# Kernel tuning notes

Measured on AMD Instinct MI355X. Metric: run time of the kernel, lower is better.

## Reference

```python
import jax, jax.numpy as jnp
import numpy as np

N_E, N_C, N_DL, N_IT, N_EP, N_HA, N_CA, N_AS = 11964, 188, 100, 7, 100, 10, 10, 7
D = 128
B, S = 256, 400
N_V = N_E + 1      # hypergraph vertices (exercises)
N_HE = N_C + 1     # hyperedges (concepts)
MEMB = 3           # concept memberships per exercise
BN_EPS = 1e-5


def _hg_v2v_mean(X, pair_v, pair_e):
    # HGNN+ smoothing: vertex -> hyperedge (mean) -> vertex (mean)
    ones_e = jnp.ones(pair_e.shape, X.dtype)
    e_deg = jnp.clip(jax.ops.segment_sum(ones_e, pair_e, num_segments=N_HE), 1.0)
    v_deg = jnp.clip(jax.ops.segment_sum(ones_e, pair_v, num_segments=N_V), 1.0)
    E = jax.ops.segment_sum(X[pair_v], pair_e, num_segments=N_HE) / e_deg[:, None]
    return jax.ops.segment_sum(E[pair_e], pair_v, num_segments=N_V) / v_deg[:, None]


def _hgnnp_conv(X, W, b, gamma, beta, mean, var, pair_v, pair_e, is_last):
    X = X @ W + b
    X = (X - mean) * jax.lax.rsqrt(var + BN_EPS) * gamma + beta  # eval-mode BN
    X = _hg_v2v_mean(X, pair_v, pair_e)
    if not is_last:
        X = jax.nn.relu(X)
    return X


def setup_inputs() -> dict:
    key = jax.random.key(0)
    ks = jax.random.split(key, 32)
    inp = {}
    inp['input_e'] = jax.random.randint(ks[0], (B, S), 0, N_V)
    inp['input_ed'] = jax.random.randint(ks[1], (B, S), 0, N_DL + 1)
    inp['input_ep'] = jax.random.randint(ks[2], (B, S), 0, N_EP + 1)
    inp['input_a'] = jax.random.randint(ks[3], (B, S), 0, 2)
    inp['input_as'] = jax.random.randint(ks[4], (B, S), 0, N_AS + 1)
    inp['input_ha'] = jax.random.randint(ks[5], (B, S), 0, N_HA + 1)
    inp['input_ca'] = jax.random.randint(ks[6], (B, S), 0, N_CA + 1)
    inp['input_it'] = jax.random.randint(ks[7], (B, S), 0, N_IT + 1)
    inp['deliver_h'] = jnp.zeros((B, D), jnp.float32)
    # hypergraph incidence (exercise-concept Q-matrix edges)
    rng = np.random.default_rng(0)
    inp['pair_v'] = jnp.asarray(np.repeat(np.arange(N_V), MEMB))
    inp['pair_e'] = jnp.asarray(rng.integers(0, N_HE, size=N_V * MEMB))
    inp['ec_map'] = jax.random.randint(ks[8], (N_V,), 0, N_HE)
    inp['ecd_map'] = jax.random.randint(ks[9], (N_V,), 0, N_DL + 1)
    # embedding tables (xavier-ish scale)
    def emb(k, n):
        return jax.random.normal(k, (n, D), jnp.float32) * 0.05
    inp['e_table'] = emb(ks[10], N_V)
    inp['c_table'] = emb(ks[11], N_HE)
    inp['ed_table'] = emb(ks[12], N_DL + 1)
    inp['cd_table'] = emb(ks[13], N_DL + 1)
    inp['a_table'] = emb(ks[14], 2)
    inp['it_table'] = emb(ks[15], N_IT + 1)
    inp['ep_table'] = emb(ks[16], N_EP + 1)
    inp['ha_table'] = emb(ks[17], N_HA + 1)
    inp['ca_table'] = emb(ks[18], N_CA + 1)
    inp['as_table'] = emb(ks[19], N_AS + 1)
    # HGNNP conv 1 & 2
    def lin(k, din, dout):
        return jax.random.normal(k, (din, dout), jnp.float32) * (1.0 / np.sqrt(din))
    inp['W1'] = lin(ks[20], D, D); inp['b1'] = jnp.zeros((D,), jnp.float32)
    inp['g1'] = jnp.ones((D,), jnp.float32); inp['be1'] = jnp.zeros((D,), jnp.float32)
    inp['m1'] = jnp.zeros((D,), jnp.float32); inp['v1'] = jnp.ones((D,), jnp.float32)
    inp['W2'] = lin(ks[21], D, D); inp['b2'] = jnp.zeros((D,), jnp.float32)
    inp['g2'] = jnp.ones((D,), jnp.float32); inp['be2'] = jnp.zeros((D,), jnp.float32)
    inp['m2'] = jnp.zeros((D,), jnp.float32); inp['v2'] = jnp.ones((D,), jnp.float32)
    # linear_i: (d_e + d_dl + d_ep + d_c + d_dl) -> d_x
    inp['Wi'] = lin(ks[22], 5 * D, D); inp['bi'] = jnp.zeros((D,), jnp.float32)
    # GRU knowledge-state cell: input = concat(x, a_emb) -> 2D, hidden D, 3 gates
    inp['Wg'] = lin(ks[23], 2 * D, 3 * D)
    inp['Ug'] = lin(ks[24], D, 3 * D)
    inp['bg'] = jnp.zeros((3 * D,), jnp.float32)
    # linear_predicting_e: d_x -> 1
    inp['We'] = lin(ks[25], D, 1); inp['beo'] = jnp.zeros((1,), jnp.float32)
    # linear_predicting_s: 4*d -> 1
    inp['Ws'] = lin(ks[26], 4 * D, 1); inp['bs'] = jnp.zeros((1,), jnp.float32)
    return inp


def reference(input_e, input_ed, input_ep, input_a, input_as, input_ha, input_ca, input_it,
              deliver_h, pair_v, pair_e, ec_map, ecd_map,
              e_table, c_table, ed_table, cd_table, a_table, it_table, ep_table,
              ha_table, ca_table, as_table,
              W1, b1, g1, be1, m1, v1, W2, b2, g2, be2, m2, v2,
              Wi, bi, Wg, Ug, bg, We, beo, Ws, bs):
    # 2-layer HGNN+ over the exercise hypergraph
    X = _hgnnp_conv(e_table, W1, b1, g1, be1, m1, v1, pair_v, pair_e, is_last=False)
    X = _hgnnp_conv(X, W2, b2, g2, be2, m2, v2, pair_v, pair_e, is_last=True)
    # embedding gathers  [B,S,D]
    e_emb = X[input_e]
    c_emb = c_table[ec_map[input_e]]
    cd_emb = cd_table[ecd_map[input_e]]
    ed_emb = ed_table[input_ed]
    ep_emb = ep_table[input_ep]
    x = jnp.tanh(jnp.concatenate([e_emb, ed_emb, ep_emb, c_emb, cd_emb], -1) @ Wi + bi)  # [B,S,D]
    a_emb = a_table[input_a]
    xs = jnp.moveaxis(jnp.concatenate([x, a_emb], -1), 1, 0)  # [S,B,2D]
    xp = jnp.moveaxis(x, 1, 0)                                # [S,B,D]

    def step(h, inputs):
        xin, xq = inputs
        y = jax.nn.sigmoid((h * xq) @ We + beo)[..., 0]  # predict from prior knowledge state
        gi = xin @ Wg + bg
        gh = h @ Ug
        iz, ir, inn = jnp.split(gi, 3, -1)
        hz, hr, hn = jnp.split(gh, 3, -1)
        z = jax.nn.sigmoid(iz + hz)
        r = jax.nn.sigmoid(ir + hr)
        n = jnp.tanh(inn + r * hn)
        return (1.0 - z) * n + z * h, y

    _, ys = jax.lax.scan(step, deliver_h, (xs, xp))
    pred_main = jnp.moveaxis(ys, 0, 1)  # [B,S]
    s_in = jnp.concatenate([ha_table[input_ha], ca_table[input_ca],
                            as_table[input_as], it_table[input_it]], -1)
    pred_s = jax.nn.sigmoid(s_in @ Ws + bs)[..., 0]  # [B,S]
    return pred_s, pred_main
```

## Files before the change

kernel.cpp:

```cpp
#include <hip/hip_runtime.h>

#define N_V   11965
#define N_HE  189
#define NPAIR 35895
#define BB    256
#define SS    400
#define DD    128
#define BSR   102400

typedef __bf16 bf16x8 __attribute__((ext_vector_type(8)));
typedef float  f32x4  __attribute__((ext_vector_type(4)));

__device__ __forceinline__ ushort f2bf(float f) {
    unsigned x = __float_as_uint(f);
    return (ushort)((x + 0x7FFFu + ((x >> 16) & 1u)) >> 16);
}
__device__ __forceinline__ float bf2f(ushort u) { return __uint_as_float(((unsigned)u) << 16); }
__device__ __forceinline__ float sigm(float x) { return 1.f / (1.f + __expf(-x)); }
__device__ __forceinline__ float tanh_f(float x) { return 2.f * sigm(2.f * x) - 1.f; }
__device__ __forceinline__ float blo(unsigned u) { return __uint_as_float(u << 16); }
__device__ __forceinline__ float bhi(unsigned u) { return __uint_as_float(u); }

struct P1Args {
    const int* pair_e;
    const float *b1, *g1, *be1, *m1, *v1;
    const float *b2, *g2, *be2, *m2, *v2;
    const float *W1, *W2, *Wi, *Wg, *Ug;
    const float *ed_t, *ep_t, *c_t, *cd_t, *a_t, *bi, *bg;
    const float *ha_t, *ca_t, *as_t, *it_t, *Ws;
    int* e_deg;
    float* aff;
    ushort *W1T, *W2T, *WiTe, *WgT, *UgT;
    float *edW, *epW, *cW, *cdW, *agi, *sd;
};

__global__ __launch_bounds__(384) void p1_kernel(P1Args A) {
    int bid = blockIdx.x, t = threadIdx.x;
    if (bid == 0) {
        if (t < 128) {
            float s = A.g1[t] * rsqrtf(A.v1[t] + 1e-5f);
            A.aff[t] = s;
            A.aff[128 + t] = A.b1[t] * s + A.be1[t] - A.m1[t] * s;
        } else if (t < 256) {
            int d = t - 128;
            float s = A.g2[d] * rsqrtf(A.v2[d] + 1e-5f);
            A.aff[256 + d] = s;
            A.aff[384 + d] = A.b2[d] * s + A.be2[d] - A.m2[d] * s;
        }
        return;
    }
    bid -= 1;
    if (bid < 94) {
        int p = bid * 384 + t;
        if (p < NPAIR) atomicAdd(&A.e_deg[A.pair_e[p]], 1);
        return;
    }
    bid -= 94;
    if (bid < 43) {
        int i = bid * 384 + t;
        if (i < 16384) { int k = i >> 7, n = i & 127; A.W1T[n * 128 + k] = f2bf(A.W1[i]); }
        return;
    }
    bid -= 43;
    if (bid < 43) {
        int i = bid * 384 + t;
        if (i < 16384) { int k = i >> 7, n = i & 127; A.W2T[n * 128 + k] = f2bf(A.W2[i]); }
        return;
    }
    bid -= 43;
    if (bid < 43) {
        int i = bid * 384 + t;
        if (i < 16384) { int k = i >> 7, n = i & 127; A.WiTe[n * 128 + k] = f2bf(A.Wi[i]); }
        return;
    }
    bid -= 43;
    if (bid < 128) {
        int i = bid * 384 + t;
        if (i < 49152) { int k = i / 384, n = i % 384; A.WgT[n * 128 + k] = f2bf(A.Wg[i]); }
        return;
    }
    bid -= 128;
    if (bid < 128) {
        int i = bid * 384 + t;
        if (i < 49152) { int k = i / 384, n = i % 384; A.UgT[n * 128 + k] = f2bf(A.Ug[i]); }
        return;
    }
    bid -= 128;
    if (bid < 101) {
        if (t < 128) {
            float acc = 0.f;
            for (int k = 0; k < 128; ++k)
                acc += A.ed_t[bid * 128 + k] * A.Wi[(128 + k) * 128 + t];
            A.edW[bid * 128 + t] = acc + A.bi[t];
        }
        return;
    }
    bid -= 101;
    if (bid < 101) {
        if (t < 128) {
            float acc = 0.f;
            for (int k = 0; k < 128; ++k)
                acc += A.ep_t[bid * 128 + k] * A.Wi[(256 + k) * 128 + t];
            A.epW[bid * 128 + t] = acc;
        }
        return;
    }
    bid -= 101;
    if (bid < 189) {
        if (t < 128) {
            float acc = 0.f;
            for (int k = 0; k < 128; ++k)
                acc += A.c_t[bid * 128 + k] * A.Wi[(384 + k) * 128 + t];
            A.cW[bid * 128 + t] = acc;
        }
        return;
    }
    bid -= 189;
    if (bid < 101) {
        if (t < 128) {
            float acc = 0.f;
            for (int k = 0; k < 128; ++k)
                acc += A.cd_t[bid * 128 + k] * A.Wi[(512 + k) * 128 + t];
            A.cdW[bid * 128 + t] = acc;
        }
        return;
    }
    bid -= 101;
    if (bid < 2) {
        float acc = 0.f;
        for (int k = 0; k < 128; ++k)
            acc += A.a_t[bid * 128 + k] * A.Wg[(128 + k) * 384 + t];
        A.agi[bid * 384 + t] = acc + A.bg[t];
        return;
    }
    bid -= 2;
    {
        int r = bid;
        const float* tab; int woff, row;
        if (r < 11)      { tab = A.ha_t; row = r;      woff = 0;   }
        else if (r < 22) { tab = A.ca_t; row = r - 11; woff = 128; }
        else if (r < 30) { tab = A.as_t; row = r - 22; woff = 256; }
        else             { tab = A.it_t; row = r - 30; woff = 384; }
        if (t < 64) {
            float p = tab[row * 128 + t] * A.Ws[woff + t]
                    + tab[row * 128 + 64 + t] * A.Ws[woff + 64 + t];
            #pragma unroll
            for (int o = 32; o > 0; o >>= 1) p += __shfl_xor(p, o);
            if (t == 0) A.sd[r] = p;
        }
    }
}

__global__ void cvt_kernel(const float* __restrict__ src, ushort* __restrict__ dst, int n) {
    int i = blockIdx.x * 256 + threadIdx.x;
    if (i < n) dst[i] = f2bf(src[i]);
}

__global__ void csr_prefix(const int* __restrict__ e_deg, int* __restrict__ start) {
    __shared__ int sc[256];
    int t = threadIdx.x;
    int d = (t < N_HE) ? e_deg[t] : 0;
    sc[t] = d;
    __syncthreads();
    for (int off = 1; off < 256; off <<= 1) {
        int v = (t >= off) ? sc[t - off] : 0;
        __syncthreads();
        sc[t] += v;
        __syncthreads();
    }
    if (t < N_HE) start[t] = sc[t] - d;
    if (t == N_HE - 1) start[N_HE] = sc[t];
}

__global__ void csr_fill(const int* __restrict__ pair_e, const int* __restrict__ pair_v,
                         const int* __restrict__ start, int* __restrict__ cursor,
                         int* __restrict__ list) {
    int p = blockIdx.x * 384 + threadIdx.x;
    if (p >= NPAIR) return;
    int e = pair_e[p];
    int pos = atomicAdd(&cursor[e], 1);
    list[start[e] + pos] = pair_v[p];
}

template <int NT>
__global__ __launch_bounds__(256) void gemm_mfma(
    const ushort* __restrict__ Amat, const ushort* __restrict__ BT,
    float* __restrict__ out, int M,
    const float* __restrict__ colS, const float* __restrict__ colB,
    const float* __restrict__ agi, const int* __restrict__ aidx) {
    const int N = NT * 16;
    int lane = threadIdx.x & 63, wave = threadIdx.x >> 6;
    int q = lane >> 4, c = lane & 15;
    int rowbase = blockIdx.x * 64 + wave * 16;
    int arow = rowbase + c;
    if (arow > M - 1) arow = M - 1;
    f32x4 acc[NT];
#pragma unroll
    for (int i = 0; i < NT; ++i) acc[i] = (f32x4){0.f, 0.f, 0.f, 0.f};
#pragma unroll
    for (int ko = 0; ko < 4; ++ko) {
        bf16x8 af = *(const bf16x8*)(Amat + (size_t)arow * 128 + ko * 32 + q * 8);
#pragma unroll
        for (int nt = 0; nt < NT; ++nt) {
            bf16x8 bfr = *(const bf16x8*)(BT + (size_t)(nt * 16 + c) * 128 + ko * 32 + q * 8);
            acc[nt] = __builtin_amdgcn_mfma_f32_16x16x32_bf16(af, bfr, acc[nt], 0, 0, 0);
        }
    }
#pragma unroll
    for (int nt = 0; nt < NT; ++nt) {
        int col = nt * 16 + c;
        float s = colS ? colS[col] : 1.f;
        float bb = colB ? colB[col] : 0.f;
#pragma unroll
        for (int r = 0; r < 4; ++r) {
            int row = rowbase + q * 4 + r;
            if (row < M) {
                float v = acc[nt][r] * s + bb;
                if (agi) v += agi[aidx[row] * N + col];
                out[(size_t)row * N + col] = v;
            }
        }
    }
}

__global__ __launch_bounds__(512) void edge_mean(const float* __restrict__ Y,
                                                 const int* __restrict__ list,
                                                 const int* __restrict__ start,
                                                 float* __restrict__ E) {
    __shared__ float red[4][128];
    int e = blockIdx.x;
    int d = threadIdx.x & 127, g = threadIdx.x >> 7;
    int s0 = start[e], n = start[e + 1] - s0;
    float acc = 0.f;
    for (int i = g; i < n; i += 4) acc += Y[(size_t)list[s0 + i] * DD + d];
    red[g][d] = acc;
    __syncthreads();
    if (g == 0) {
        float v = red[0][d] + red[1][d] + red[2][d] + red[3][d];
        E[e * DD + d] = v / (float)(n > 0 ? n : 1);
    }
}

__global__ void v_mean(const float* __restrict__ E, const int* __restrict__ pair_e,
                       ushort* __restrict__ Xo, int relu) {
    int idx = blockIdx.x * 256 + threadIdx.x;
    if (idx >= N_V * DD) return;
    int v = idx >> 7, d = idx & 127;
    float a = E[pair_e[3 * v] * DD + d] + E[pair_e[3 * v + 1] * DD + d] +
              E[pair_e[3 * v + 2] * DD + d];
    a *= (1.f / 3.f);
    if (relu) a = fmaxf(a, 0.f);
    Xo[idx] = f2bf(a);
}

__global__ void k3_kernel(const int* __restrict__ in_e, const int* __restrict__ in_ed,
                          const int* __restrict__ in_ep, const float* __restrict__ XW,
                          const float* __restrict__ cW, const float* __restrict__ cdW,
                          const float* __restrict__ edW, const float* __restrict__ epW,
                          const int* __restrict__ ec_map, const int* __restrict__ ecd_map,
                          ushort* __restrict__ xbf) {
    int idx = blockIdx.x * 256 + threadIdx.x;
    if (idx >= BSR * DD) return;
    int row = idx >> 7, d = idx & 127;
    int e = in_e[row];
    float v = XW[(size_t)e * DD + d] + cW[ec_map[e] * DD + d] + cdW[ecd_map[e] * DD + d] +
              edW[in_ed[row] * DD + d] + epW[in_ep[row] * DD + d];
    xbf[idx] = f2bf(tanh_f(v));
}

__global__ void pred_s_kernel(const int* __restrict__ ha, const int* __restrict__ ca,
                              const int* __restrict__ as_, const int* __restrict__ it,
                              const float* __restrict__ sd, const float* __restrict__ bs,
                              float* __restrict__ out) {
    int i = blockIdx.x * 256 + threadIdx.x;
    if (i >= BSR) return;
    float v = sd[ha[i]] + sd[11 + ca[i]] + sd[22 + as_[i]] + sd[30 + it[i]] + bs[0];
    out[i] = sigm(v);
}

__global__ void
__attribute__((amdgpu_flat_work_group_size(768, 768), amdgpu_waves_per_eu(2, 3)))
gru_scan(
    const float* __restrict__ gi, const ushort* __restrict__ xb,
    const ushort* __restrict__ UgT, const float* __restrict__ h0,
    const float* __restrict__ We, const float* __restrict__ beo_p,
    float* __restrict__ out) {
    __shared__ __align__(16) float h_s[128];
    __shared__ float pp[4][392];
    __shared__ float n_sL[128];
    __shared__ float p_s[128];
    int b = blockIdx.x, t = threadIdx.x;
    int kq = t / 192;
    int cp = t % 192;
    const unsigned* WA = (const unsigned*)(UgT + (size_t)cp * 128 + kq * 32);
    const unsigned* WB = (const unsigned*)(UgT + (size_t)(cp + 192) * 128 + kq * 32);
    unsigned a0 = WA[0], a1 = WA[1], a2 = WA[2], a3 = WA[3], a4 = WA[4], a5 = WA[5],
             a6 = WA[6], a7 = WA[7], a8 = WA[8], a9 = WA[9], a10 = WA[10], a11 = WA[11],
             a12 = WA[12], a13 = WA[13], a14 = WA[14], a15 = WA[15];
    unsigned c0 = WB[0], c1 = WB[1], c2 = WB[2], c3 = WB[3], c4 = WB[4], c5 = WB[5],
             c6 = WB[6], c7 = WB[7], c8 = WB[8], c9 = WB[9], c10 = WB[10], c11 = WB[11],
             c12 = WB[12], c13 = WB[13], c14 = WB[14], c15 = WB[15];
    float beo = beo_p[0];
    float wev = 0.f;
    if (t < 128) { wev = We[t]; h_s[t] = h0[b * 128 + t]; }
    const float* gip = gi + (size_t)b * SS * 384;
    const ushort* xp = xb + (size_t)b * SS * 128;
    float gz_nx = 0.f, gr_nx = 0.f, gn_nx = 0.f, xw_nx = 0.f;
    if (t < 128) {
        gz_nx = gip[t];
        xw_nx = bf2f(xp[t]) * wev;
    } else if (t >= 256 && t < 384) {
        gr_nx = gip[t - 128];
        gn_nx = gip[t];
    }
    float* omain = out + BSR + b * SS;
    __syncthreads();
    for (int s = 0; s < SS; ++s) {
#define PIN(X) asm volatile("" : "+v"(X));
        PIN(a0) PIN(a1) PIN(a2) PIN(a3) PIN(a4) PIN(a5) PIN(a6) PIN(a7)
        PIN(a8) PIN(a9) PIN(a10) PIN(a11) PIN(a12) PIN(a13) PIN(a14) PIN(a15)
        PIN(c0) PIN(c1) PIN(c2) PIN(c3) PIN(c4) PIN(c5) PIN(c6) PIN(c7)
        PIN(c8) PIN(c9) PIN(c10) PIN(c11) PIN(c12) PIN(c13) PIN(c14) PIN(c15)
#undef PIN
        float gz = gz_nx, gr = gr_nx, gn = gn_nx, xw = xw_nx;
        if (s + 1 < SS) {
            const float* g2 = gip + (size_t)(s + 1) * 384;
            if (t < 128) {
                gz_nx = g2[t];
                xw_nx = bf2f(xp[(size_t)(s + 1) * 128 + t]) * wev;
            } else if (t >= 256 && t < 384) {
                gr_nx = g2[t - 128];
                gn_nx = g2[t];
            }
        }
        const float4* h4 = (const float4*)h_s + kq * 8;
        float accA = 0.f, accB = 0.f;
#define FB(I, UL, UH, VL, VH) { float4 hv = h4[I]; \
        accA = fmaf(hv.x, blo(UL), accA); accA = fmaf(hv.y, bhi(UL), accA); \
        accA = fmaf(hv.z, blo(UH), accA); accA = fmaf(hv.w, bhi(UH), accA); \
        accB = fmaf(hv.x, blo(VL), accB); accB = fmaf(hv.y, bhi(VL), accB); \
        accB = fmaf(hv.z, blo(VH), accB); accB = fmaf(hv.w, bhi(VH), accB); }
        FB(0, a0, a1, c0, c1)    FB(1, a2, a3, c2, c3)
        FB(2, a4, a5, c4, c5)    FB(3, a6, a7, c6, c7)
        FB(4, a8, a9, c8, c9)    FB(5, a10, a11, c10, c11)
        FB(6, a12, a13, c12, c13) FB(7, a14, a15, c14, c15)
#undef FB
        pp[kq][cp] = accA;
        pp[kq][cp + 192] = accB;
        __syncthreads();
        float z = 0.f, h_old = 0.f;
        if (t < 128) {
            float S = pp[0][t] + pp[1][t] + pp[2][t] + pp[3][t];
            z = sigm(gz + S);
            h_old = h_s[t];
            p_s[t] = h_old * xw;
        } else if (t >= 256 && t < 384) {
            int j = t - 256;
            float Sr = pp[0][128 + j] + pp[1][128 + j] + pp[2][128 + j] + pp[3][128 + j];
            float Sn = pp[0][256 + j] + pp[1][256 + j] + pp[2][256 + j] + pp[3][256 + j];
            float r = sigm(gr + Sr);
            n_sL[j] = tanh_f(gn + r * Sn);
        }
        __syncthreads();
        if (t < 128) {
            h_s[t] = (1.f - z) * n_sL[t] + z * h_old;
        } else if (t >= 384 && t < 448) {
            int l = t - 384;
            float pv = p_s[l] + p_s[l + 64];
#pragma unroll
            for (int o = 32; o > 0; o >>= 1) pv += __shfl_xor(pv, o);
            if (l == 0) omain[s] = sigm(pv + beo);
        }
        __syncthreads();
    }
}

extern "C" void kernel_launch(void* const* d_in, const int* in_sizes, int n_in,
                              void* d_out, int out_size, void* d_ws, size_t ws_size,
                              hipStream_t stream) {
    const int* in_e   = (const int*)d_in[0];
    const int* in_ed  = (const int*)d_in[1];
    const int* in_ep  = (const int*)d_in[2];
    const int* in_a   = (const int*)d_in[3];
    const int* in_as  = (const int*)d_in[4];
    const int* in_ha  = (const int*)d_in[5];
    const int* in_ca  = (const int*)d_in[6];
    const int* in_it  = (const int*)d_in[7];
    const float* deliver_h = (const float*)d_in[8];
    const int* pair_v = (const int*)d_in[9];
    const int* pair_e = (const int*)d_in[10];
    const int* ec_map = (const int*)d_in[11];
    const int* ecd_map= (const int*)d_in[12];
    const float* e_table  = (const float*)d_in[13];
    const float* c_table  = (const float*)d_in[14];
    const float* ed_table = (const float*)d_in[15];
    const float* cd_table = (const float*)d_in[16];
    const float* a_table  = (const float*)d_in[17];
    const float* it_table = (const float*)d_in[18];
    const float* ep_table = (const float*)d_in[19];
    const float* ha_table = (const float*)d_in[20];
    const float* ca_table = (const float*)d_in[21];
    const float* as_table = (const float*)d_in[22];
    const float* W1 = (const float*)d_in[23];
    const float* b1 = (const float*)d_in[24];
    const float* g1 = (const float*)d_in[25];
    const float* be1= (const float*)d_in[26];
    const float* m1 = (const float*)d_in[27];
    const float* v1 = (const float*)d_in[28];
    const float* W2 = (const float*)d_in[29];
    const float* b2 = (const float*)d_in[30];
    const float* g2 = (const float*)d_in[31];
    const float* be2= (const float*)d_in[32];
    const float* m2 = (const float*)d_in[33];
    const float* v2 = (const float*)d_in[34];
    const float* Wi = (const float*)d_in[35];
    const float* bi = (const float*)d_in[36];
    const float* Wg = (const float*)d_in[37];
    const float* Ug = (const float*)d_in[38];
    const float* bg = (const float*)d_in[39];
    const float* We = (const float*)d_in[40];
    const float* beo= (const float*)d_in[41];
    const float* Ws = (const float*)d_in[42];
    const float* bs = (const float*)d_in[43];
    float* out = (float*)d_out;
    char* ws = (char*)d_ws;

    size_t off = 0;
    auto alloc = [&](size_t bytes) { size_t o = off; off += (bytes + 255) & ~(size_t)255; return o; };
    size_t o_degcur = alloc(378 * 4);
    size_t o_start  = alloc(190 * 4);
    size_t o_list   = alloc((size_t)NPAIR * 4);
    size_t o_aff    = alloc(512 * 4);
    size_t o_W1T    = alloc(16384 * 2);
    size_t o_W2T    = alloc(16384 * 2);
    size_t o_WiTe   = alloc(16384 * 2);
    size_t o_WgT    = alloc(49152 * 2);
    size_t o_UgT    = alloc(49152 * 2);
    size_t o_edW    = alloc(101 * 128 * 4);
    size_t o_epW    = alloc(101 * 128 * 4);
    size_t o_cW     = alloc(189 * 128 * 4);
    size_t o_cdW    = alloc(101 * 128 * 4);
    size_t o_agi    = alloc(2 * 384 * 4);
    size_t o_sd     = alloc(38 * 4);
    size_t o_etb    = alloc((size_t)N_V * DD * 2);
    size_t o_E      = alloc((size_t)N_HE * DD * 4);
    size_t o_Y      = alloc((size_t)N_V * DD * 4);
    size_t o_X1     = alloc((size_t)N_V * DD * 2);
    size_t o_X2     = alloc((size_t)N_V * DD * 2);
    size_t o_XW     = alloc((size_t)N_V * DD * 4);
    size_t o_xbf    = alloc((size_t)BSR * DD * 2);
    size_t o_gi     = alloc((size_t)BSR * 384 * 4);

    int*    e_deg  = (int*)(ws + o_degcur);
    int*    cursor = e_deg + 189;
    int*    startp = (int*)(ws + o_start);
    int*    listp  = (int*)(ws + o_list);
    float*  aff    = (float*)(ws + o_aff);
    ushort* W1T    = (ushort*)(ws + o_W1T);
    ushort* W2T    = (ushort*)(ws + o_W2T);
    ushort* WiTe   = (ushort*)(ws + o_WiTe);
    ushort* WgT    = (ushort*)(ws + o_WgT);
    ushort* UgTp   = (ushort*)(ws + o_UgT);
    float*  edW    = (float*)(ws + o_edW);
    float*  epW    = (float*)(ws + o_epW);
    float*  cW     = (float*)(ws + o_cW);
    float*  cdW    = (float*)(ws + o_cdW);
    float*  agi    = (float*)(ws + o_agi);
    float*  sd     = (float*)(ws + o_sd);
    ushort* e_tb   = (ushort*)(ws + o_etb);
    float*  E      = (float*)(ws + o_E);
    float*  Y      = (float*)(ws + o_Y);
    ushort* X1b    = (ushort*)(ws + o_X1);
    ushort* X2b    = (ushort*)(ws + o_X2);
    float*  XW     = (float*)(ws + o_XW);
    ushort* xbf    = (ushort*)(ws + o_xbf);
    float*  gi     = (float*)(ws + o_gi);

    hipMemsetAsync(ws + o_degcur, 0, 378 * 4, stream);

    P1Args pa;
    pa.pair_e = pair_e;
    pa.b1 = b1; pa.g1 = g1; pa.be1 = be1; pa.m1 = m1; pa.v1 = v1;
    pa.b2 = b2; pa.g2 = g2; pa.be2 = be2; pa.m2 = m2; pa.v2 = v2;
    pa.W1 = W1; pa.W2 = W2; pa.Wi = Wi; pa.Wg = Wg; pa.Ug = Ug;
    pa.ed_t = ed_table; pa.ep_t = ep_table; pa.c_t = c_table; pa.cd_t = cd_table;
    pa.a_t = a_table; pa.bi = bi; pa.bg = bg;
    pa.ha_t = ha_table; pa.ca_t = ca_table; pa.as_t = as_table; pa.it_t = it_table; pa.Ws = Ws;
    pa.e_deg = e_deg; pa.aff = aff;
    pa.W1T = W1T; pa.W2T = W2T; pa.WiTe = WiTe; pa.WgT = WgT; pa.UgT = UgTp;
    pa.edW = edW; pa.epW = epW; pa.cW = cW; pa.cdW = cdW; pa.agi = agi; pa.sd = sd;
    p1_kernel<<<1012, 384, 0, stream>>>(pa);

    cvt_kernel<<<(N_V * DD + 255) / 256, 256, 0, stream>>>(e_table, e_tb, N_V * DD);
    csr_prefix<<<1, 256, 0, stream>>>(e_deg, startp);
    csr_fill<<<94, 384, 0, stream>>>(pair_e, pair_v, startp, cursor, listp);

    pred_s_kernel<<<(BSR + 255) / 256, 256, 0, stream>>>(in_ha, in_ca, in_as, in_it, sd, bs, out);

    gemm_mfma<8><<<(N_V + 63) / 64, 256, 0, stream>>>(e_tb, W1T, Y, N_V, aff, aff + 128,
                                                      nullptr, nullptr);
    edge_mean<<<N_HE, 512, 0, stream>>>(Y, listp, startp, E);
    v_mean<<<(N_V * DD + 255) / 256, 256, 0, stream>>>(E, pair_e, X1b, 1);
    gemm_mfma<8><<<(N_V + 63) / 64, 256, 0, stream>>>(X1b, W2T, Y, N_V, aff + 256, aff + 384,
                                                      nullptr, nullptr);
    edge_mean<<<N_HE, 512, 0, stream>>>(Y, listp, startp, E);
    v_mean<<<(N_V * DD + 255) / 256, 256, 0, stream>>>(E, pair_e, X2b, 0);
    gemm_mfma<8><<<(N_V + 63) / 64, 256, 0, stream>>>(X2b, WiTe, XW, N_V, nullptr, nullptr,
                                                      nullptr, nullptr);
    k3_kernel<<<(BSR * DD + 255) / 256, 256, 0, stream>>>(in_e, in_ed, in_ep, XW, cW, cdW, edW,
                                                          epW, ec_map, ecd_map, xbf);
    gemm_mfma<24><<<BSR / 64, 256, 0, stream>>>(xbf, WgT, gi, BSR, nullptr, nullptr, agi, in_a);
    gru_scan<<<BB, 768, 0, stream>>>(gi, xbf, UgTp, deliver_h, We, beo, out);
}
```

Before: 1.011 ms.

## Stage GRU recurrent weights in padded LDS instead of pinned registers

```diff
diff --git a/kernel.cpp b/kernel.cpp
--- a/kernel.cpp
+++ b/kernel.cpp
@@ -278,28 +278,34 @@
     out[i] = sigm(v);
 }
 
+#define WLDS_BYTES (384 * 272)
+#define GRU_LDS_BYTES (WLDS_BYTES + (128 * 3 + 4 * 392) * 4)
+
 __global__ void
-__attribute__((amdgpu_flat_work_group_size(768, 768), amdgpu_waves_per_eu(2, 3)))
-gru_scan(
+__attribute__((amdgpu_flat_work_group_size(768, 768)))
+gru_scan_lds(
     const float* __restrict__ gi, const ushort* __restrict__ xb,
     const ushort* __restrict__ UgT, const float* __restrict__ h0,
     const float* __restrict__ We, const float* __restrict__ beo_p,
     float* __restrict__ out) {
-    __shared__ __align__(16) float h_s[128];
-    __shared__ float pp[4][392];
-    __shared__ float n_sL[128];
-    __shared__ float p_s[128];
+    extern __shared__ __align__(16) char smem[];
+    ushort* w_lds = (ushort*)smem;
+    float* h_s  = (float*)(smem + WLDS_BYTES);
+    float* p_s  = h_s + 128;
+    float* n_sL = p_s + 128;
+    float* pp   = n_sL + 128;
     int b = blockIdx.x, t = threadIdx.x;
     int kq = t / 192;
     int cp = t % 192;
-    const unsigned* WA = (const unsigned*)(UgT + (size_t)cp * 128 + kq * 32);
-    const unsigned* WB = (const unsigned*)(UgT + (size_t)(cp + 192) * 128 + kq * 32);
-    unsigned a0 = WA[0], a1 = WA[1], a2 = WA[2], a3 = WA[3], a4 = WA[4], a5 = WA[5],
-             a6 = WA[6], a7 = WA[7], a8 = WA[8], a9 = WA[9], a10 = WA[10], a11 = WA[11],
-             a12 = WA[12], a13 = WA[13], a14 = WA[14], a15 = WA[15];
-    unsigned c0 = WB[0], c1 = WB[1], c2 = WB[2], c3 = WB[3], c4 = WB[4], c5 = WB[5],
-             c6 = WB[6], c7 = WB[7], c8 = WB[8], c9 = WB[9], c10 = WB[10], c11 = WB[11],
-             c12 = WB[12], c13 = WB[13], c14 = WB[14], c15 = WB[15];
+#pragma unroll
+    for (int j = 0; j < 8; ++j) {
+        int idx = j * 768 + t;
+        uint4 v = ((const uint4*)UgT)[idx];
+        int c = idx >> 4, u = idx & 15;
+        ((uint4*)w_lds)[c * 17 + u] = v;
+    }
+    const uint4* wA = (const uint4*)w_lds + cp * 17 + kq * 4;
+    const uint4* wB = (const uint4*)w_lds + (cp + 192) * 17 + kq * 4;
     float beo = beo_p[0];
     float wev = 0.f;
     if (t < 128) { wev = We[t]; h_s[t] = h0[b * 128 + t]; }
@@ -316,12 +322,6 @@
     float* omain = out + BSR + b * SS;
     __syncthreads();
     for (int s = 0; s < SS; ++s) {
-#define PIN(X) asm volatile("" : "+v"(X));
-        PIN(a0) PIN(a1) PIN(a2) PIN(a3) PIN(a4) PIN(a5) PIN(a6) PIN(a7)
-        PIN(a8) PIN(a9) PIN(a10) PIN(a11) PIN(a12) PIN(a13) PIN(a14) PIN(a15)
-        PIN(c0) PIN(c1) PIN(c2) PIN(c3) PIN(c4) PIN(c5) PIN(c6) PIN(c7)
-        PIN(c8) PIN(c9) PIN(c10) PIN(c11) PIN(c12) PIN(c13) PIN(c14) PIN(c15)
-#undef PIN
         float gz = gz_nx, gr = gr_nx, gn = gn_nx, xw = xw_nx;
         if (s + 1 < SS) {
             const float* g2 = gip + (size_t)(s + 1) * 384;
@@ -335,16 +335,109 @@
         }
         const float4* h4 = (const float4*)h_s + kq * 8;
         float accA = 0.f, accB = 0.f;
-#define FB(I, UL, UH, VL, VH) { float4 hv = h4[I]; \
-        accA = fmaf(hv.x, blo(UL), accA); accA = fmaf(hv.y, bhi(UL), accA); \
-        accA = fmaf(hv.z, blo(UH), accA); accA = fmaf(hv.w, bhi(UH), accA); \
-        accB = fmaf(hv.x, blo(VL), accB); accB = fmaf(hv.y, bhi(VL), accB); \
-        accB = fmaf(hv.z, blo(VH), accB); accB = fmaf(hv.w, bhi(VH), accB); }
-        FB(0, a0, a1, c0, c1)    FB(1, a2, a3, c2, c3)
-        FB(2, a4, a5, c4, c5)    FB(3, a6, a7, c6, c7)
-        FB(4, a8, a9, c8, c9)    FB(5, a10, a11, c10, c11)
-        FB(6, a12, a13, c12, c13) FB(7, a14, a15, c14, c15)
-#undef FB
+#pragma unroll
+        for (int i = 0; i < 4; ++i) {
+            uint4 a = wA[i];
+            uint4 c = wB[i];
+            float4 hv0 = h4[2 * i], hv1 = h4[2 * i + 1];
+            accA = fmaf(hv0.x, blo(a.x), accA); accA = fmaf(hv0.y, bhi(a.x), accA);
+            accA = fmaf(hv0.z, blo(a.y), accA); accA = fmaf(hv0.w, bhi(a.y), accA);
+            accA = fmaf(hv1.x, blo(a.z), accA); accA = fmaf(hv1.y, bhi(a.z), accA);
+            accA = fmaf(hv1.z, blo(a.w), accA); accA = fmaf(hv1.w, bhi(a.w), accA);
+            accB = fmaf(hv0.x, blo(c.x), accB); accB = fmaf(hv0.y, bhi(c.x), accB);
+            accB = fmaf(hv0.z, blo(c.y), accB); accB = fmaf(hv0.w, bhi(c.y), accB);
+            accB = fmaf(hv1.x, blo(c.z), accB); accB = fmaf(hv1.y, bhi(c.z), accB);
+            accB = fmaf(hv1.z, blo(c.w), accB); accB = fmaf(hv1.w, bhi(c.w), accB);
+        }
+        pp[kq * 392 + cp] = accA;
+        pp[kq * 392 + cp + 192] = accB;
+        __syncthreads();
+        float z = 0.f, h_old = 0.f;
+        if (t < 128) {
+            float S = pp[t] + pp[392 + t] + pp[784 + t] + pp[1176 + t];
+            z = sigm(gz + S);
+            h_old = h_s[t];
+            p_s[t] = h_old * xw;
+        } else if (t >= 256 && t < 384) {
+            int j = t - 256;
+            float Sr = pp[128 + j] + pp[392 + 128 + j] + pp[784 + 128 + j] + pp[1176 + 128 + j];
+            float Sn = pp[256 + j] + pp[392 + 256 + j] + pp[784 + 256 + j] + pp[1176 + 256 + j];
+            float r = sigm(gr + Sr);
+            n_sL[j] = tanh_f(gn + r * Sn);
+        }
+        __syncthreads();
+        if (t < 128) {
+            h_s[t] = (1.f - z) * n_sL[t] + z * h_old;
+        } else if (t >= 384 && t < 448) {
+            int l = t - 384;
+            float pv = p_s[l] + p_s[l + 64];
+#pragma unroll
+            for (int o = 32; o > 0; o >>= 1) pv += __shfl_xor(pv, o);
+            if (l == 0) omain[s] = sigm(pv + beo);
+        }
+        __syncthreads();
+    }
+}
+
+__global__ void
+__attribute__((amdgpu_flat_work_group_size(768, 768)))
+gru_scan_glob(
+    const float* __restrict__ gi, const ushort* __restrict__ xb,
+    const ushort* __restrict__ UgT, const float* __restrict__ h0,
+    const float* __restrict__ We, const float* __restrict__ beo_p,
+    float* __restrict__ out) {
+    __shared__ __align__(16) float h_s[128];
+    __shared__ float pp[4][392];
+    __shared__ float n_sL[128];
+    __shared__ float p_s[128];
+    int b = blockIdx.x, t = threadIdx.x;
+    int kq = t / 192;
+    int cp = t % 192;
+    const uint4* WA = (const uint4*)(UgT + (size_t)cp * 128 + kq * 32);
+    const uint4* WB = (const uint4*)(UgT + (size_t)(cp + 192) * 128 + kq * 32);
+    float beo = beo_p[0];
+    float wev = 0.f;
+    if (t < 128) { wev = We[t]; h_s[t] = h0[b * 128 + t]; }
+    const float* gip = gi + (size_t)b * SS * 384;
+    const ushort* xp = xb + (size_t)b * SS * 128;
+    float gz_nx = 0.f, gr_nx = 0.f, gn_nx = 0.f, xw_nx = 0.f;
+    if (t < 128) {
+        gz_nx = gip[t];
+        xw_nx = bf2f(xp[t]) * wev;
+    } else if (t >= 256 && t < 384) {
+        gr_nx = gip[t - 128];
+        gn_nx = gip[t];
+    }
+    float* omain = out + BSR + b * SS;
+    __syncthreads();
+    for (int s = 0; s < SS; ++s) {
+        float gz = gz_nx, gr = gr_nx, gn = gn_nx, xw = xw_nx;
+        if (s + 1 < SS) {
+            const float* g2 = gip + (size_t)(s + 1) * 384;
+            if (t < 128) {
+                gz_nx = g2[t];
+                xw_nx = bf2f(xp[(size_t)(s + 1) * 128 + t]) * wev;
+            } else if (t >= 256 && t < 384) {
+                gr_nx = g2[t - 128];
+                gn_nx = g2[t];
+            }
+        }
+        const float4* h4 = (const float4*)h_s + kq * 8;
+        float accA = 0.f, accB = 0.f;
+#pragma unroll
+        for (int i = 0; i < 4; ++i) {
+            uint4 a = WA[i];
+            uint4 c = WB[i];
+            float4 hv0 = h4[2 * i], hv1 = h4[2 * i + 1];
+            accA = fmaf(hv0.x, blo(a.x), accA); accA = fmaf(hv0.y, bhi(a.x), accA);
+            accA = fmaf(hv0.z, blo(a.y), accA); accA = fmaf(hv0.w, bhi(a.y), accA);
+            accA = fmaf(hv1.x, blo(a.z), accA); accA = fmaf(hv1.y, bhi(a.z), accA);
+            accA = fmaf(hv1.z, blo(a.w), accA); accA = fmaf(hv1.w, bhi(a.w), accA);
+            accB = fmaf(hv0.x, blo(c.x), accB); accB = fmaf(hv0.y, bhi(c.x), accB);
+            accB = fmaf(hv0.z, blo(c.y), accB); accB = fmaf(hv0.w, bhi(c.y), accB);
+            accB = fmaf(hv1.x, blo(c.z), accB); accB = fmaf(hv1.y, bhi(c.z), accB);
+            accB = fmaf(hv1.z, blo(c.w), accB); accB = fmaf(hv1.w, bhi(c.w), accB);
+        }
         pp[kq][cp] = accA;
         pp[kq][cp + 192] = accB;
         __syncthreads();
@@ -510,5 +603,13 @@
     k3_kernel<<<(BSR * DD + 255) / 256, 256, 0, stream>>>(in_e, in_ed, in_ep, XW, cW, cdW, edW,
                                                           epW, ec_map, ecd_map, xbf);
     gemm_mfma<24><<<BSR / 64, 256, 0, stream>>>(xbf, WgT, gi, BSR, nullptr, nullptr, agi, in_a);
-    gru_scan<<<BB, 768, 0, stream>>>(gi, xbf, UgTp, deliver_h, We, beo, out);
-}
+
+    hipError_t attr_ok = hipFuncSetAttribute(
+        reinterpret_cast<const void*>(gru_scan_lds),
+        hipFuncAttributeMaxDynamicSharedMemorySize, GRU_LDS_BYTES);
+    if (attr_ok == hipSuccess) {
+        gru_scan_lds<<<BB, 768, GRU_LDS_BYTES, stream>>>(gi, xbf, UgTp, deliver_h, We, beo, out);
+    } else {
+        gru_scan_glob<<<BB, 768, 0, stream>>>(gi, xbf, UgTp, deliver_h, We, beo, out);
+    }
+}
```

After: 1.031 ms. About the same (+1.9%).

## Cut GRU scan barriers per step and pin weights in AGPRs

Applied to the files above, without the earlier changes.

```diff
diff --git a/kernel.cpp b/kernel.cpp
--- a/kernel.cpp
+++ b/kernel.cpp
@@ -279,99 +279,109 @@
 }
 
 __global__ void
-__attribute__((amdgpu_flat_work_group_size(768, 768), amdgpu_waves_per_eu(2, 3)))
+__attribute__((amdgpu_flat_work_group_size(768, 768)))
 gru_scan(
     const float* __restrict__ gi, const ushort* __restrict__ xb,
     const ushort* __restrict__ UgT, const float* __restrict__ h0,
     const float* __restrict__ We, const float* __restrict__ beo_p,
     float* __restrict__ out) {
     __shared__ __align__(16) float h_s[128];
+    __shared__ float p_s[128];
     __shared__ float pp[4][392];
-    __shared__ float n_sL[128];
-    __shared__ float p_s[128];
     int b = blockIdx.x, t = threadIdx.x;
     int kq = t / 192;
     int cp = t % 192;
-    const unsigned* WA = (const unsigned*)(UgT + (size_t)cp * 128 + kq * 32);
-    const unsigned* WB = (const unsigned*)(UgT + (size_t)(cp + 192) * 128 + kq * 32);
-    unsigned a0 = WA[0], a1 = WA[1], a2 = WA[2], a3 = WA[3], a4 = WA[4], a5 = WA[5],
-             a6 = WA[6], a7 = WA[7], a8 = WA[8], a9 = WA[9], a10 = WA[10], a11 = WA[11],
-             a12 = WA[12], a13 = WA[13], a14 = WA[14], a15 = WA[15];
-    unsigned c0 = WB[0], c1 = WB[1], c2 = WB[2], c3 = WB[3], c4 = WB[4], c5 = WB[5],
-             c6 = WB[6], c7 = WB[7], c8 = WB[8], c9 = WB[9], c10 = WB[10], c11 = WB[11],
-             c12 = WB[12], c13 = WB[13], c14 = WB[14], c15 = WB[15];
+    const uint4* WA = (const uint4*)(UgT + (size_t)cp * 128 + kq * 32);
+    const uint4* WB = (const uint4*)(UgT + (size_t)(cp + 192) * 128 + kq * 32);
+    uint4 A0 = WA[0], A1 = WA[1], A2 = WA[2], A3 = WA[3];
+    uint4 B0 = WB[0], B1 = WB[1], B2 = WB[2], B3 = WB[3];
+    unsigned a0 = A0.x, a1 = A0.y, a2 = A0.z, a3 = A0.w;
+    unsigned a4 = A1.x, a5 = A1.y, a6 = A1.z, a7 = A1.w;
+    unsigned a8 = A2.x, a9 = A2.y, a10 = A2.z, a11 = A2.w;
+    unsigned a12 = A3.x, a13 = A3.y, a14 = A3.z, a15 = A3.w;
+    unsigned c0 = B0.x, c1 = B0.y, c2 = B0.z, c3 = B0.w;
+    unsigned c4 = B1.x, c5 = B1.y, c6 = B1.z, c7 = B1.w;
+    unsigned c8 = B2.x, c9 = B2.y, c10 = B2.z, c11 = B2.w;
+    unsigned c12 = B3.x, c13 = B3.y, c14 = B3.z, c15 = B3.w;
     float beo = beo_p[0];
-    float wev = 0.f;
-    if (t < 128) { wev = We[t]; h_s[t] = h0[b * 128 + t]; }
+    float wev = 0.f, hreg = 0.f;
+    if (t < 128) {
+        wev = We[t];
+        hreg = h0[b * 128 + t];
+        h_s[t] = hreg;
+    }
     const float* gip = gi + (size_t)b * SS * 384;
     const ushort* xp = xb + (size_t)b * SS * 128;
     float gz_nx = 0.f, gr_nx = 0.f, gn_nx = 0.f, xw_nx = 0.f;
     if (t < 128) {
         gz_nx = gip[t];
+        gr_nx = gip[128 + t];
+        gn_nx = gip[256 + t];
         xw_nx = bf2f(xp[t]) * wev;
-    } else if (t >= 256 && t < 384) {
-        gr_nx = gip[t - 128];
-        gn_nx = gip[t];
     }
     float* omain = out + BSR + b * SS;
     __syncthreads();
     for (int s = 0; s < SS; ++s) {
-#define PIN(X) asm volatile("" : "+v"(X));
-        PIN(a0) PIN(a1) PIN(a2) PIN(a3) PIN(a4) PIN(a5) PIN(a6) PIN(a7)
-        PIN(a8) PIN(a9) PIN(a10) PIN(a11) PIN(a12) PIN(a13) PIN(a14) PIN(a15)
-        PIN(c0) PIN(c1) PIN(c2) PIN(c3) PIN(c4) PIN(c5) PIN(c6) PIN(c7)
-        PIN(c8) PIN(c9) PIN(c10) PIN(c11) PIN(c12) PIN(c13) PIN(c14) PIN(c15)
-#undef PIN
+#define PINA(X) asm volatile("" : "+a"(X));
+        PINA(a0) PINA(a1) PINA(a2) PINA(a3) PINA(a4) PINA(a5) PINA(a6) PINA(a7)
+        PINA(a8) PINA(a9) PINA(a10) PINA(a11) PINA(a12) PINA(a13) PINA(a14) PINA(a15)
+        PINA(c0) PINA(c1) PINA(c2) PINA(c3) PINA(c4) PINA(c5) PINA(c6) PINA(c7)
+        PINA(c8) PINA(c9) PINA(c10) PINA(c11) PINA(c12) PINA(c13) PINA(c14) PINA(c15)
+#undef PINA
         float gz = gz_nx, gr = gr_nx, gn = gn_nx, xw = xw_nx;
-        if (s + 1 < SS) {
+        if (s + 1 < SS && t < 128) {
             const float* g2 = gip + (size_t)(s + 1) * 384;
-            if (t < 128) {
-                gz_nx = g2[t];
-                xw_nx = bf2f(xp[(size_t)(s + 1) * 128 + t]) * wev;
-            } else if (t >= 256 && t < 384) {
-                gr_nx = g2[t - 128];
-                gn_nx = g2[t];
-            }
+            gz_nx = g2[t];
+            gr_nx = g2[128 + t];
+            gn_nx = g2[256 + t];
+            xw_nx = bf2f(xp[(size_t)(s + 1) * 128 + t]) * wev;
         }
         const float4* h4 = (const float4*)h_s + kq * 8;
         float accA = 0.f, accB = 0.f;
-#define FB(I, UL, UH, VL, VH) { float4 hv = h4[I]; \
-        accA = fmaf(hv.x, blo(UL), accA); accA = fmaf(hv.y, bhi(UL), accA); \
-        accA = fmaf(hv.z, blo(UH), accA); accA = fmaf(hv.w, bhi(UH), accA); \
-        accB = fmaf(hv.x, blo(VL), accB); accB = fmaf(hv.y, bhi(VL), accB); \
-        accB = fmaf(hv.z, blo(VH), accB); accB = fmaf(hv.w, bhi(VH), accB); }
-        FB(0, a0, a1, c0, c1)    FB(1, a2, a3, c2, c3)
-        FB(2, a4, a5, c4, c5)    FB(3, a6, a7, c6, c7)
-        FB(4, a8, a9, c8, c9)    FB(5, a10, a11, c10, c11)
-        FB(6, a12, a13, c12, c13) FB(7, a14, a15, c14, c15)
-#undef FB
+#define FB2(HI, U0, U1, U2, U3, V0, V1, V2, V3) { \
+        float4 hv0 = h4[HI], hv1 = h4[HI + 1]; \
+        accA = fmaf(hv0.x, blo(U0), accA); accA = fmaf(hv0.y, bhi(U0), accA); \
+        accA = fmaf(hv0.z, blo(U1), accA); accA = fmaf(hv0.w, bhi(U1), accA); \
+        accA = fmaf(hv1.x, blo(U2), accA); accA = fmaf(hv1.y, bhi(U2), accA); \
+        accA = fmaf(hv1.z, blo(U3), accA); accA = fmaf(hv1.w, bhi(U3), accA); \
+        accB = fmaf(hv0.x, blo(V0), accB); accB = fmaf(hv0.y, bhi(V0), accB); \
+        accB = fmaf(hv0.z, blo(V1), accB); accB = fmaf(hv0.w, bhi(V1), accB); \
+        accB = fmaf(hv1.x, blo(V2), accB); accB = fmaf(hv1.y, bhi(V2), accB); \
+        accB = fmaf(hv1.z, blo(V3), accB); accB = fmaf(hv1.w, bhi(V3), accB); }
+        FB2(0, a0, a1, a2, a3, c0, c1, c2, c3)
+        FB2(2, a4, a5, a6, a7, c4, c5, c6, c7)
+        FB2(4, a8, a9, a10, a11, c8, c9, c10, c11)
+        FB2(6, a12, a13, a14, a15, c12, c13, c14, c15)
+#undef FB2
         pp[kq][cp] = accA;
         pp[kq][cp + 192] = accB;
-        __syncthreads();
-        float z = 0.f, h_old = 0.f;
-        if (t < 128) {
-            float S = pp[0][t] + pp[1][t] + pp[2][t] + pp[3][t];
-            z = sigm(gz + S);
-            h_old = h_s[t];
-            p_s[t] = h_old * xw;
-        } else if (t >= 256 && t < 384) {
-            int j = t - 256;
-            float Sr = pp[0][128 + j] + pp[1][128 + j] + pp[2][128 + j] + pp[3][128 + j];
-            float Sn = pp[0][256 + j] + pp[1][256 + j] + pp[2][256 + j] + pp[3][256 + j];
-            float r = sigm(gr + Sr);
-            n_sL[j] = tanh_f(gn + r * Sn);
+        if (t >= 704 && s > 0) {
+            int l = t - 704;
+            float pv = p_s[l] + p_s[l + 64];
+#pragma unroll
+            for (int o = 32; o > 0; o >>= 1) pv += __shfl_xor(pv, o);
+            if (l == 0) omain[s - 1] = sigm(pv + beo);
         }
         __syncthreads();
         if (t < 128) {
-            h_s[t] = (1.f - z) * n_sL[t] + z * h_old;
-        } else if (t >= 384 && t < 448) {
-            int l = t - 384;
-            float pv = p_s[l] + p_s[l + 64];
-#pragma unroll
-            for (int o = 32; o > 0; o >>= 1) pv += __shfl_xor(pv, o);
-            if (l == 0) omain[s] = sigm(pv + beo);
+            float Sz = pp[0][t] + pp[1][t] + pp[2][t] + pp[3][t];
+            float Sr = pp[0][128 + t] + pp[1][128 + t] + pp[2][128 + t] + pp[3][128 + t];
+            float Sn = pp[0][256 + t] + pp[1][256 + t] + pp[2][256 + t] + pp[3][256 + t];
+            float z = sigm(gz + Sz);
+            float r = sigm(gr + Sr);
+            float n = tanh_f(gn + r * Sn);
+            p_s[t] = hreg * xw;
+            hreg = (1.f - z) * n + z * hreg;
+            h_s[t] = hreg;
         }
         __syncthreads();
+    }
+    if (t >= 704) {
+        int l = t - 704;
+        float pv = p_s[l] + p_s[l + 64];
+#pragma unroll
+        for (int o = 32; o > 0; o >>= 1) pv += __shfl_xor(pv, o);
+        if (l == 0) omain[SS - 1] = sigm(pv + beo);
     }
 }
 
```

After: 976.5 us. 3.4% less time.
